# Optimization experiments

Measured on AMD Instinct MI355X. Metric: run time of the kernel, lower is better.

Reference implementation:

```python
import jax, jax.numpy as jnp
import numpy as np

N, E, B = 10000, 25000, 128
NF, EF, D = 32, 8, 64
STEPS = 3   # message passing steps
S2S = 3     # set2set processing steps
EPS = 1e-5

def setup_inputs() -> dict:
    key = jax.random.key(0)
    ks = jax.random.split(key, 32)
    g = lambda i, shape, scale=0.05: (jax.random.normal(ks[i], shape, dtype=jnp.float32) * scale)
    inp = {
        'x': jax.random.normal(ks[0], (N, NF), dtype=jnp.float32),
        'edge_index': jax.random.randint(ks[1], (2, E), 0, N, dtype=jnp.int32),
        'edge_attr': jax.random.normal(ks[2], (E, EF), dtype=jnp.float32),
        'batch': jnp.sort(jax.random.randint(ks[3], (N,), 0, B, dtype=jnp.int32)),
        # dense0
        'W0': g(4, (NF, D)), 'b0': jnp.zeros((D,), jnp.float32),
        # edge MLP: EF -> 2D -> D*D
        'We1': g(5, (EF, 2 * D)), 'be1': jnp.zeros((2 * D,), jnp.float32),
        'We2': g(6, (2 * D, D * D)), 'be2': jnp.zeros((D * D,), jnp.float32),
        # NNConv root weight + bias
        'root': g(7, (D, D)), 'conv_b': jnp.zeros((D,), jnp.float32),
        # GRU (input D, hidden D); gate order r, z, n (torch layout)
        'Wi': g(8, (D, 3 * D)), 'bi': jnp.zeros((3 * D,), jnp.float32),
        'Wh': g(9, (D, 3 * D)), 'bh': jnp.zeros((3 * D,), jnp.float32),
        # Set2Set LSTM (input 2D, hidden D); gate order i, f, g, o
        'Wli': g(10, (2 * D, 4 * D)), 'bli': jnp.zeros((4 * D,), jnp.float32),
        'Wlh': g(11, (D, 4 * D)), 'blh': jnp.zeros((4 * D,), jnp.float32),
        'Wr1': g(12, (2 * D, D)), 'br1': jnp.zeros((D,), jnp.float32),
        'gamma': jnp.ones((D,), jnp.float32), 'beta': jnp.zeros((D,), jnp.float32),
        'Wr2': g(13, (D, 1)), 'br2': jnp.zeros((1,), jnp.float32),
    }
    return inp

def _forward(x, edge_index, edge_attr, batch, W0, b0, We1, be1, We2, be2,
             root, conv_b, Wi, bi, Wh, bh, Wli, bli, Wlh, blh,
             Wr1, br1, gamma, beta, Wr2, br2):
    src, dst = edge_index[0], edge_index[1]
    out = jax.nn.relu(x @ W0 + b0)            # [N, D]
    h = out                                    # GRU hidden (seq_len=1)
    # edge-conditioned weights depend only on edge_attr -> compute once
    ew = (jax.nn.relu(edge_attr @ We1 + be1) @ We2 + be2).reshape(E, D, D)
    deg = jnp.maximum(jax.ops.segment_sum(jnp.ones((E,), x.dtype), dst, num_segments=N), 1.0)
    for _ in range(STEPS):
        msg = jnp.einsum('ed,edf->ef', out[src], ew)               # [E, D]
        agg = jax.ops.segment_sum(msg, dst, num_segments=N) / deg[:, None]
        m = jax.nn.relu(agg + out @ root + conv_b)                  # NNConv + relu
        # GRU cell
        gi = m @ Wi + bi
        gh = h @ Wh + bh
        ir, iz, ig = jnp.split(gi, 3, axis=-1)
        hr, hz, hg = jnp.split(gh, 3, axis=-1)
        r = jax.nn.sigmoid(ir + hr)
        z = jax.nn.sigmoid(iz + hz)
        n = jnp.tanh(ig + r * hg)
        h = (1.0 - z) * n + z * h
        out = h
    # Set2Set readout
    q_star = jnp.zeros((B, 2 * D), x.dtype)
    hl = jnp.zeros((B, D), x.dtype)
    cl = jnp.zeros((B, D), x.dtype)
    for _ in range(S2S):
        gates = q_star @ Wli + bli + hl @ Wlh + blh
        ig_, fg_, gg_, og_ = jnp.split(gates, 4, axis=-1)
        cl = jax.nn.sigmoid(fg_) * cl + jax.nn.sigmoid(ig_) * jnp.tanh(gg_)
        hl = jax.nn.sigmoid(og_) * jnp.tanh(cl)
        q = hl                                                      # [B, D]
        e = jnp.sum(out * q[batch], axis=-1)                        # [N]
        emax = jax.ops.segment_max(e, batch, num_segments=B)
        a = jnp.exp(e - emax[batch])
        a = a / jnp.maximum(jax.ops.segment_sum(a, batch, num_segments=B), 1e-12)[batch]
        r_read = jax.ops.segment_sum(a[:, None] * out, batch, num_segments=B)  # [B, D]
        q_star = jnp.concatenate([q, r_read], axis=-1)
    y = q_star @ Wr1 + br1
    mu = jnp.mean(y, axis=0)
    var = jnp.mean((y - mu) ** 2, axis=0)
    y = (y - mu) * jax.lax.rsqrt(var + EPS) * gamma + beta
    y = jax.nn.relu(y)
    y = y @ Wr2 + br2
    return y.reshape(-1)                                            # [B]

def reference(x, edge_index, edge_attr, batch, W0, b0, We1, be1, We2, be2,
              root, conv_b, Wi, bi, Wh, bh, Wli, bli, Wlh, blh,
              Wr1, br1, gamma, beta, Wr2, br2):
    return _forward(x, edge_index, edge_attr, batch, W0, b0, We1, be1, We2, be2,
                    root, conv_b, Wi, bi, Wh, bh, Wli, bli, Wlh, blh,
                    Wr1, br1, gamma, beta, Wr2, br2)
```

## Files before the change

kernel.cpp:

```cpp
#include <hip/hip_runtime.h>
#include <hip/hip_bf16.h>

constexpr int kN = 10000;
constexpr int kE = 25000;
constexpr int kB = 128;
constexpr int kNF = 32;
constexpr int kEF = 8;
constexpr int kD = 64;
constexpr int kGrp = 392;
constexpr int kEPad = kGrp * 64;
constexpr int kNCap = 320;

typedef __attribute__((ext_vector_type(8))) short short8;
typedef __attribute__((ext_vector_type(4))) float floatx4;
typedef __attribute__((ext_vector_type(16))) float floatx16;

__device__ __forceinline__ unsigned short f2bf(float f) {
  unsigned u = __float_as_uint(f);
  u = (u + 0x7fffu + ((u >> 16) & 1u)) >> 16;
  return (unsigned short)u;
}
__device__ __forceinline__ float sigmf(float x) { return 1.f / (1.f + __expf(-x)); }
__device__ __forceinline__ float tanh_(float x) { return 1.f - 2.f / (__expf(2.f * x) + 1.f); }

__device__ __forceinline__ unsigned cvtpk(float lo, float hi) {
  unsigned r;
  asm("v_cvt_pk_bf16_f32 %0, %1, %2" : "=v"(r) : "v"(lo), "v"(hi));
  return r;
}

constexpr int kBlkDense = 2500;
constexpr int kBlkHid   = 12544;
constexpr int kBlkPrep  = 258;
constexpr int kBlkDeg   = 98;
constexpr int kB0H = kBlkDense;
constexpr int kB0P = kB0H + kBlkHid;
constexpr int kB0G = kB0P + kBlkPrep;
constexpr int kB0B = kB0G + kBlkDeg;
constexpr int kBlkSetup = kB0B + 1;

__global__ __launch_bounds__(256) void k_setup(
    const float* __restrict__ x, const float* __restrict__ W0, const float* __restrict__ b0,
    const float* __restrict__ ea, const float* __restrict__ We1, const float* __restrict__ be1,
    const float* __restrict__ We2, const float* __restrict__ be2,
    const int* __restrict__ ei, const int* __restrict__ batch,
    float* __restrict__ outn, unsigned short* __restrict__ hid7,
    unsigned short* __restrict__ Bc2, float* __restrict__ deg, int* __restrict__ start) {
  const int blk = blockIdx.x, t = threadIdx.x;
  if (blk < kB0H) {
    int gid = blk * 256 + t;
    int n = gid >> 6, f = gid & 63;
    float acc = b0[f];
    const float* xr = x + n * kNF;
#pragma unroll
    for (int j = 0; j < kNF; ++j) acc += xr[j] * W0[j * kD + f];
    outn[gid] = fmaxf(acc, 0.f);
  } else if (blk < kB0P) {
    int gid = (blk - kB0H) * 256 + t;
    int e_loc = gid & 63, h = (gid >> 6) & 127, grp = gid >> 13;
    int e = grp * 64 + e_loc;
    float r = 0.f;
    if (e < kE) {
      float acc = be1[h];
      const float* er = ea + e * kEF;
#pragma unroll
      for (int j = 0; j < kEF; ++j) acc += er[j] * We1[j * 128 + h];
      r = fmaxf(acc, 0.f);
    }
    hid7[gid] = f2bf(r);
  } else if (blk < kB0G) {
    int lg = (blk - kB0P) * 256 + t;
    int lane = lg & 63, slot = lg >> 6;
    int fcol, dbase;
    const float* srcmat;
    if (slot < 1024) {
      int nf_ = slot & 1, hdb = slot >> 1;
      int db = hdb & 3, h = hdb >> 2;
      fcol = nf_ * 32 + (lane & 31);
      dbase = db * 16 + (lane >> 5) * 8;
      srcmat = We2 + (size_t)h * 4096;
    } else {
      int s = slot - 1024;
      int db = s >> 1, nf_ = s & 1;
      fcol = nf_ * 32 + (lane & 31);
      dbase = db * 16 + (lane >> 5) * 8;
      srcmat = be2;
    }
    unsigned short v[8];
#pragma unroll
    for (int j = 0; j < 8; ++j) v[j] = f2bf(srcmat[(size_t)(dbase + j) * 64 + fcol]);
    *(short8*)(Bc2 + (size_t)slot * 512 + lane * 8) = *(short8*)v;
  } else if (blk < kB0B) {
    int e = (blk - kB0G) * 256 + t;
    if (e < kE) atomicAdd(&deg[ei[kE + e]], 1.f);
  } else {
    if (t > kB) return;
    int lo = 0, hi = kN;
    while (lo < hi) { int mid = (lo + hi) >> 1; if (batch[mid] < t) lo = mid + 1; else hi = mid; }
    start[t] = lo;
  }
}

__global__ __launch_bounds__(256) void k_csr(const float* __restrict__ deg,
                                             int* __restrict__ ptr) {
  __shared__ int ps[256];
  int t = threadIdx.x;
  int base = t * 40;
  int s = 0;
#pragma unroll 8
  for (int j = 0; j < 40; ++j) {
    int n = base + j;
    if (n < kN) s += (int)deg[n];
  }
  ps[t] = s;
  __syncthreads();
  for (int off = 1; off < 256; off <<= 1) {
    int v = (t >= off) ? ps[t - off] : 0;
    __syncthreads();
    ps[t] += v;
    __syncthreads();
  }
  int run = ps[t] - s;
  for (int j = 0; j < 40; ++j) {
    int n = base + j;
    if (n < kN) { ptr[n] = run; run += (int)deg[n]; }
  }
  if (t == 255) ptr[kN] = ps[255];
}

__global__ __launch_bounds__(256) void k_scatter(const int* __restrict__ ei,
    const int* __restrict__ ptr, int* __restrict__ cnt, int* __restrict__ csr) {
  int e = blockIdx.x * 256 + threadIdx.x;
  if (e < kE) {
    int d = ei[kE + e];
    int pos = atomicAdd(&cnt[d], 1);
    csr[ptr[d] + pos] = e;
  }
}

__global__ __launch_bounds__(256) void k_msg7(const int* __restrict__ ei,
    const float* __restrict__ outn, const unsigned short* __restrict__ hid7,
    const unsigned short* __restrict__ Bc2,
    float* __restrict__ msg0, float* __restrict__ msg1) {
  __shared__ __align__(16) unsigned short hidS[64 * 64];
  __shared__ __align__(16) float res[4][64 * 64];
  const int t = threadIdx.x, lane = t & 63, wave = t >> 6;
  const int er = lane & 31, hi5 = lane >> 5;
  const int grp = blockIdx.x, by = blockIdx.y, e0 = grp * 64;
  float* __restrict__ msgP = by ? msg1 : msg0;
  {
    const char* hsrc = (const char*)(hid7 + (size_t)grp * 8192 + by * 4096);
#pragma unroll
    for (int i = 0; i < 2; ++i) {
      int off = (wave * 2 + i) * 1024 + lane * 16;
      __builtin_amdgcn_global_load_lds(
          (const __attribute__((address_space(1))) void*)(hsrc + off),
          (__attribute__((address_space(3))) void*)((char*)hidS + off), 16, 0, 0);
    }
  }
  const int hg0 = by * 64 + wave * 16;
  const unsigned short* bp = Bc2 + (size_t)(hg0 * 8) * 512 + lane * 8;
  short8 bvr[8];
#pragma unroll
  for (int j = 0; j < 8; ++j) bvr[j] = *(const short8*)(bp + (size_t)j * 512);
  floatx4 o[2][4][2];
#pragma unroll
  for (int mf = 0; mf < 2; ++mf) {
    int e = e0 + mf * 32 + er;
    int s = (e < kE) ? ei[e] : 0;
    const float* base = outn + (size_t)s * 64 + hi5 * 8;
#pragma unroll
    for (int db = 0; db < 4; ++db) {
      o[mf][db][0] = *(const floatx4*)(base + db * 16);
      o[mf][db][1] = *(const floatx4*)(base + db * 16 + 4);
    }
  }
  __syncthreads();

  floatx16 acc[2][2];
#pragma unroll
  for (int mf = 0; mf < 2; ++mf)
#pragma unroll
    for (int nf = 0; nf < 2; ++nf)
#pragma unroll
      for (int i = 0; i < 16; ++i) acc[mf][nf][i] = 0.f;

  const int hl0 = wave * 16;
#pragma unroll 2
  for (int hh = 0; hh < 16; ++hh) {
    int hl = hl0 + hh;
    float hv0 = __uint_as_float(((unsigned)hidS[hl * 64 + er]) << 16);
    float hv1 = __uint_as_float(((unsigned)hidS[hl * 64 + 32 + er]) << 16);
    const unsigned short* bpn = bp + (size_t)((hh + 1) * 8) * 512;
#pragma unroll
    for (int db = 0; db < 4; ++db) {
      short8 bv0 = bvr[db * 2], bv1 = bvr[db * 2 + 1];
      bvr[db * 2]     = *(const short8*)(bpn + (size_t)(db * 2) * 512);
      bvr[db * 2 + 1] = *(const short8*)(bpn + (size_t)(db * 2 + 1) * 512);
      union { uint4 u; short8 s; } U0, U1;
      floatx4 a0 = o[0][db][0] * hv0, b0 = o[0][db][1] * hv0;
      floatx4 a1 = o[1][db][0] * hv1, b1 = o[1][db][1] * hv1;
      U0.u.x = cvtpk(a0.x, a0.y); U0.u.y = cvtpk(a0.z, a0.w);
      U0.u.z = cvtpk(b0.x, b0.y); U0.u.w = cvtpk(b0.z, b0.w);
      U1.u.x = cvtpk(a1.x, a1.y); U1.u.y = cvtpk(a1.z, a1.w);
      U1.u.z = cvtpk(b1.x, b1.y); U1.u.w = cvtpk(b1.z, b1.w);
      acc[0][0] = __builtin_amdgcn_mfma_f32_32x32x16_bf16(U0.s, bv0, acc[0][0], 0, 0, 0);
      acc[0][1] = __builtin_amdgcn_mfma_f32_32x32x16_bf16(U0.s, bv1, acc[0][1], 0, 0, 0);
      acc[1][0] = __builtin_amdgcn_mfma_f32_32x32x16_bf16(U1.s, bv0, acc[1][0], 0, 0, 0);
      acc[1][1] = __builtin_amdgcn_mfma_f32_32x32x16_bf16(U1.s, bv1, acc[1][1], 0, 0, 0);
    }
  }
  if (by == 1 && wave == 3) {
#pragma unroll
    for (int db = 0; db < 4; ++db) {
      short8 bv0 = *(const short8*)(Bc2 + (size_t)(1024 + db * 2) * 512 + lane * 8);
      short8 bv1 = *(const short8*)(Bc2 + (size_t)(1024 + db * 2 + 1) * 512 + lane * 8);
      union { uint4 u; short8 s; } U0, U1;
      floatx4 a0 = o[0][db][0], b0 = o[0][db][1];
      floatx4 a1 = o[1][db][0], b1 = o[1][db][1];
      U0.u.x = cvtpk(a0.x, a0.y); U0.u.y = cvtpk(a0.z, a0.w);
      U0.u.z = cvtpk(b0.x, b0.y); U0.u.w = cvtpk(b0.z, b0.w);
      U1.u.x = cvtpk(a1.x, a1.y); U1.u.y = cvtpk(a1.z, a1.w);
      U1.u.z = cvtpk(b1.x, b1.y); U1.u.w = cvtpk(b1.z, b1.w);
      acc[0][0] = __builtin_amdgcn_mfma_f32_32x32x16_bf16(U0.s, bv0, acc[0][0], 0, 0, 0);
      acc[0][1] = __builtin_amdgcn_mfma_f32_32x32x16_bf16(U0.s, bv1, acc[0][1], 0, 0, 0);
      acc[1][0] = __builtin_amdgcn_mfma_f32_32x32x16_bf16(U1.s, bv0, acc[1][0], 0, 0, 0);
      acc[1][1] = __builtin_amdgcn_mfma_f32_32x32x16_bf16(U1.s, bv1, acc[1][1], 0, 0, 0);
    }
  }
#pragma unroll
  for (int mf = 0; mf < 2; ++mf)
#pragma unroll
    for (int nf = 0; nf < 2; ++nf)
#pragma unroll
      for (int reg = 0; reg < 16; ++reg) {
        int row = (reg & 3) + 8 * (reg >> 2) + 4 * hi5 + mf * 32;
        res[wave][row * 64 + nf * 32 + er] = acc[mf][nf][reg];
      }
  __syncthreads();
#pragma unroll
  for (int q = 0; q < 4; ++q) {
    int idx = q * 1024 + t * 4;
    float4 s4 = *(const float4*)&res[0][idx];
#pragma unroll
    for (int w = 1; w < 4; ++w) {
      float4 a4 = *(const float4*)&res[w][idx];
      s4.x += a4.x; s4.y += a4.y; s4.z += a4.z; s4.w += a4.w;
    }
    int e = e0 + (idx >> 6);
    if (e < kE) *(float4*)(msgP + (size_t)e * 64 + (idx & 63)) = s4;
  }
}

__global__ __launch_bounds__(256) void k_update(const float* __restrict__ msg0,
    const float* __restrict__ msg1, const int* __restrict__ ptr,
    const int* __restrict__ csr, const float* __restrict__ deg,
    const float* __restrict__ root, const float* __restrict__ convb,
    const float* __restrict__ Wi, const float* __restrict__ bi,
    const float* __restrict__ Wh, const float* __restrict__ bh,
    float* __restrict__ out) {
  __shared__ float sh_out[16][64];
  __shared__ float sh_m[16][64];
  int t = threadIdx.x, lane = t & 63, w = t >> 6;
  int nb = blockIdx.x * 16;
#pragma unroll
  for (int i = 0; i < 4; ++i) {
    int idx = t + i * 256;
    sh_out[idx >> 6][idx & 63] = out[(size_t)(nb + (idx >> 6)) * 64 + (idx & 63)];
  }
  __syncthreads();
  int n0 = w * 4;
  float acc[4];
#pragma unroll
  for (int i = 0; i < 4; ++i) {
    int n = nb + n0 + i;
    float dg = fmaxf(deg[n], 1.f);
    float s = 0.f;
    int p0 = ptr[n], p1 = ptr[n + 1];
    for (int k = p0; k < p1; ++k) {
      size_t off2 = (size_t)csr[k] * 64 + lane;
      s += msg0[off2] + msg1[off2];
    }
    acc[i] = s / dg + convb[lane];
  }
  for (int d = 0; d < 64; ++d) {
    float rv = root[d * 64 + lane];
#pragma unroll
    for (int i = 0; i < 4; ++i) acc[i] += sh_out[n0 + i][d] * rv;
  }
#pragma unroll
  for (int i = 0; i < 4; ++i) sh_m[n0 + i][lane] = fmaxf(acc[i], 0.f);
  __syncthreads();
  float ir[4] = {}, iz[4] = {}, ig[4] = {}, hr[4] = {}, hz[4] = {}, hg[4] = {};
  for (int d = 0; d < 64; ++d) {
    float wi0 = Wi[d * 192 + lane], wi1 = Wi[d * 192 + 64 + lane], wi2 = Wi[d * 192 + 128 + lane];
    float wh0 = Wh[d * 192 + lane], wh1 = Wh[d * 192 + 64 + lane], wh2 = Wh[d * 192 + 128 + lane];
#pragma unroll
    for (int i = 0; i < 4; ++i) {
      float mv = sh_m[n0 + i][d], hv = sh_out[n0 + i][d];
      ir[i] += mv * wi0; iz[i] += mv * wi1; ig[i] += mv * wi2;
      hr[i] += hv * wh0; hz[i] += hv * wh1; hg[i] += hv * wh2;
    }
  }
  float bi0 = bi[lane], bi1 = bi[64 + lane], bi2 = bi[128 + lane];
  float bh0 = bh[lane], bh1 = bh[64 + lane], bh2 = bh[128 + lane];
#pragma unroll
  for (int i = 0; i < 4; ++i) {
    float r = sigmf(ir[i] + bi0 + hr[i] + bh0);
    float z = sigmf(iz[i] + bi1 + hz[i] + bh1);
    float nn = tanh_(ig[i] + bi2 + r * (hg[i] + bh2));
    float h = sh_out[n0 + i][lane];
    out[(size_t)(nb + n0 + i) * 64 + lane] = (1.f - z) * nn + z * h;
  }
}

__global__ __launch_bounds__(256) void k_s2s3(const float* __restrict__ out,
    const int* __restrict__ start, const float* __restrict__ Wli,
    const float* __restrict__ bli, const float* __restrict__ Wlh,
    const float* __restrict__ blh, const float* __restrict__ Wr1,
    const float* __restrict__ br1, float* __restrict__ y1) {
  __shared__ float sno[kNCap * 65];
  __shared__ float ebuf[1024];
  __shared__ float qs[128], hls[64], cls[64], gates[256];
  __shared__ float part[4][64];
  __shared__ float sred[8];
  int b = blockIdx.x, t = threadIdx.x, lane = t & 63, w = t >> 6;
  int s0 = start[b], s1 = start[b + 1];
  int cnt = s1 - s0; if (cnt > 1024) cnt = 1024;
  int cstg = cnt < kNCap ? cnt : kNCap;
  for (int i = t; i < cstg * 64; i += 256)
    sno[(i >> 6) * 65 + (i & 63)] = out[(size_t)(s0 + (i >> 6)) * 64 + (i & 63)];
  if (t < 128) qs[t] = 0.f;
  if (t < 64) { hls[t] = 0.f; cls[t] = 0.f; }
  __syncthreads();
  for (int it = 0; it < 3; ++it) {
    float g = bli[t] + blh[t];
    for (int j = 0; j < 128; ++j) g += qs[j] * Wli[j * 256 + t];
    for (int j = 0; j < 64; ++j) g += hls[j] * Wlh[j * 256 + t];
    gates[t] = g;
    __syncthreads();
    if (t < 64) {
      float ig = sigmf(gates[t]), fg = sigmf(gates[64 + t]);
      float gg = tanh_(gates[128 + t]), og = sigmf(gates[192 + t]);
      float c = fg * cls[t] + ig * gg;
      float h = og * tanh_(c);
      cls[t] = c; hls[t] = h;
      qs[t] = h;
    }
    __syncthreads();
    for (int n = t; n < cnt; n += 256) {
      float e = 0.f;
      if (n < kNCap) {
        const float* row = &sno[n * 65];
#pragma unroll 16
        for (int d = 0; d < 64; ++d) e += row[d] * hls[d];
      } else {
        const float* row = out + (size_t)(s0 + n) * 64;
        for (int d = 0; d < 64; ++d) e += row[d] * hls[d];
      }
      ebuf[n] = e;
    }
    __syncthreads();
    float mx = -3.4e38f;
    for (int idx = t; idx < cnt; idx += 256) mx = fmaxf(mx, ebuf[idx]);
#pragma unroll
    for (int m = 1; m < 64; m <<= 1) mx = fmaxf(mx, __shfl_xor(mx, m, 64));
    if (lane == 0) sred[w] = mx;
    __syncthreads();
    mx = fmaxf(fmaxf(sred[0], sred[1]), fmaxf(sred[2], sred[3]));
    float s = 0.f;
    for (int idx = t; idx < cnt; idx += 256) {
      float a = __expf(ebuf[idx] - mx);
      ebuf[idx] = a; s += a;
    }
#pragma unroll
    for (int m = 1; m < 64; m <<= 1) s += __shfl_xor(s, m, 64);
    if (lane == 0) sred[4 + w] = s;
    __syncthreads();
    s = sred[4] + sred[5] + sred[6] + sred[7];
    float rs = 1.f / fmaxf(s, 1e-12f);
    float pr = 0.f;
    for (int n = w; n < cnt; n += 4) {
      float a = ebuf[n];
      pr += a * ((n < kNCap) ? sno[n * 65 + lane] : out[(size_t)(s0 + n) * 64 + lane]);
    }
    part[w][lane] = pr;
    __syncthreads();
    if (t < 64)
      qs[64 + t] = (part[0][t] + part[1][t] + part[2][t] + part[3][t]) * rs;
    __syncthreads();
  }
  if (t < 64) {
    float acc = br1[t];
    for (int j = 0; j < 128; ++j) acc += qs[j] * Wr1[j * 64 + t];
    y1[b * 64 + t] = acc;
  }
}

__global__ __launch_bounds__(256) void k_head2(const float* __restrict__ y1,
    const float* __restrict__ gamma, const float* __restrict__ beta,
    const float* __restrict__ Wr2, const float* __restrict__ br2,
    float* __restrict__ outp) {
  __shared__ float mu[64], ri[64];
  int t = threadIdx.x;
  if (t < 64) {
    float s1 = 0.f, s2 = 0.f;
    for (int b = 0; b < kB; ++b) { float v = y1[b * 64 + t]; s1 += v; s2 += v * v; }
    float m = s1 / (float)kB;
    mu[t] = m; ri[t] = rsqrtf(s2 / (float)kB - m * m + 1e-5f);
  }
  __syncthreads();
  if (t < kB) {
    float acc = br2[0];
    for (int f = 0; f < 64; ++f) {
      float v = (y1[t * 64 + f] - mu[f]) * ri[f] * gamma[f] + beta[f];
      acc += fmaxf(v, 0.f) * Wr2[f];
    }
    outp[t] = acc;
  }
}

extern "C" void kernel_launch(void* const* d_in, const int* in_sizes, int n_in,
                              void* d_out, int out_size, void* d_ws, size_t ws_size,
                              hipStream_t stream) {
  const float* x     = (const float*)d_in[0];
  const int*   ei    = (const int*)d_in[1];
  const float* ea    = (const float*)d_in[2];
  const int*   batch = (const int*)d_in[3];
  const float* W0    = (const float*)d_in[4];
  const float* b0    = (const float*)d_in[5];
  const float* We1   = (const float*)d_in[6];
  const float* be1   = (const float*)d_in[7];
  const float* We2   = (const float*)d_in[8];
  const float* be2   = (const float*)d_in[9];
  const float* root  = (const float*)d_in[10];
  const float* convb = (const float*)d_in[11];
  const float* Wi    = (const float*)d_in[12];
  const float* bi    = (const float*)d_in[13];
  const float* Wh    = (const float*)d_in[14];
  const float* bh    = (const float*)d_in[15];
  const float* Wli   = (const float*)d_in[16];
  const float* bli   = (const float*)d_in[17];
  const float* Wlh   = (const float*)d_in[18];
  const float* blh   = (const float*)d_in[19];
  const float* Wr1   = (const float*)d_in[20];
  const float* br1   = (const float*)d_in[21];
  const float* gamma = (const float*)d_in[22];
  const float* beta  = (const float*)d_in[23];
  const float* Wr2   = (const float*)d_in[24];
  const float* br2   = (const float*)d_in[25];
  (void)in_sizes; (void)n_in; (void)out_size; (void)ws_size;

  char* ws = (char*)d_ws;
  size_t off = 0;
  auto take = [&](size_t bytes) {
    char* p = ws + off;
    off += (bytes + 255) & ~(size_t)255;
    return p;
  };
  float* deg  = (float*)take((size_t)kN * 4);
  int*   cnt  = (int*)take((size_t)kN * 4);
  size_t zeroBytes = off;
  int*   ptr   = (int*)take((size_t)(kN + 1) * 4);
  int*   csr   = (int*)take((size_t)kE * 4);
  int*   start = (int*)take(256 * 4);
  float* outn  = (float*)take((size_t)kN * kD * 4);
  float* msg0  = (float*)take((size_t)kEPad * kD * 4);
  float* msg1  = (float*)take((size_t)kEPad * kD * 4);
  unsigned short* hid7 = (unsigned short*)take((size_t)kGrp * 8192 * 2);
  unsigned short* Bc2  = (unsigned short*)take((size_t)1032 * 512 * 2);
  float* y1    = (float*)take((size_t)kB * 64 * 4);

  hipMemsetAsync(deg, 0, zeroBytes, stream);
  k_setup<<<kBlkSetup, 256, 0, stream>>>(x, W0, b0, ea, We1, be1, We2, be2, ei, batch,
                                         outn, hid7, Bc2, deg, start);
  k_csr<<<1, 256, 0, stream>>>(deg, ptr);
  k_scatter<<<(kE + 255) / 256, 256, 0, stream>>>(ei, ptr, cnt, csr);
  dim3 gm(kGrp, 2);
  for (int s = 0; s < 3; ++s) {
    k_msg7<<<gm, 256, 0, stream>>>(ei, outn, hid7, Bc2, msg0, msg1);
    k_update<<<kN / 16, 256, 0, stream>>>(msg0, msg1, ptr, csr, deg, root, convb,
                                          Wi, bi, Wh, bh, outn);
  }
  k_s2s3<<<kB, 256, 0, stream>>>(outn, start, Wli, bli, Wlh, blh, Wr1, br1, y1);
  k_head2<<<1, 256, 0, stream>>>(y1, gamma, beta, Wr2, br2, (float*)d_out);
}
```

Before: 284.5 us.

## Switch edge-message MFMA to fp16 with packed half multiply and halve reduction LDS

The edge-message kernel now stores hidden activations and the We2/be2 tiles in fp16 instead of bf16. Source node features are converted to packed fp16 once, outside the loop, and each per-hidden scaling is a single packed half8 multiply rather than fp32 multiplies followed by bf16 pack conversions, which feeds f16 MFMA. The cross-wave reduction buffer is cut to half size by reducing the two 32-edge halves in sequence with extra barriers. Together these are meant to cut VALU conversion work in the inner loop and raise occupancy through lower LDS use, at the cost of fp16 range and rounding risks (round-toward-zero packing, products computed in half precision).

```diff
diff --git a/kernel.cpp b/kernel.cpp
--- a/kernel.cpp
+++ b/kernel.cpp
@@ -14,20 +14,22 @@
 typedef __attribute__((ext_vector_type(8))) short short8;
 typedef __attribute__((ext_vector_type(4))) float floatx4;
 typedef __attribute__((ext_vector_type(16))) float floatx16;
-
-__device__ __forceinline__ unsigned short f2bf(float f) {
-  unsigned u = __float_as_uint(f);
-  u = (u + 0x7fffu + ((u >> 16) & 1u)) >> 16;
-  return (unsigned short)u;
+typedef _Float16 half8 __attribute__((ext_vector_type(8)));
+
+union HU { uint4 u; half8 h; short8 s; };
+
+__device__ __forceinline__ unsigned short f2h(float f) {
+  union { _Float16 h; unsigned short u; } cv;
+  cv.h = (_Float16)f;
+  return cv.u;
+}
+__device__ __forceinline__ unsigned pkrtz(float lo, float hi) {
+  unsigned r;
+  asm("v_cvt_pkrtz_f16_f32 %0, %1, %2" : "=v"(r) : "v"(lo), "v"(hi));
+  return r;
 }
 __device__ __forceinline__ float sigmf(float x) { return 1.f / (1.f + __expf(-x)); }
 __device__ __forceinline__ float tanh_(float x) { return 1.f - 2.f / (__expf(2.f * x) + 1.f); }
-
-__device__ __forceinline__ unsigned cvtpk(float lo, float hi) {
-  unsigned r;
-  asm("v_cvt_pk_bf16_f32 %0, %1, %2" : "=v"(r) : "v"(lo), "v"(hi));
-  return r;
-}
 
 constexpr int kBlkDense = 2500;
 constexpr int kBlkHid   = 12544;
@@ -67,7 +69,7 @@
       for (int j = 0; j < kEF; ++j) acc += er[j] * We1[j * 128 + h];
       r = fmaxf(acc, 0.f);
     }
-    hid7[gid] = f2bf(r);
+    hid7[gid] = f2h(r);
   } else if (blk < kB0G) {
     int lg = (blk - kB0P) * 256 + t;
     int lane = lg & 63, slot = lg >> 6;
@@ -88,7 +90,7 @@
     }
     unsigned short v[8];
 #pragma unroll
-    for (int j = 0; j < 8; ++j) v[j] = f2bf(srcmat[(size_t)(dbase + j) * 64 + fcol]);
+    for (int j = 0; j < 8; ++j) v[j] = f2h(srcmat[(size_t)(dbase + j) * 64 + fcol]);
     *(short8*)(Bc2 + (size_t)slot * 512 + lane * 8) = *(short8*)v;
   } else if (blk < kB0B) {
     int e = (blk - kB0G) * 256 + t;
@@ -138,12 +140,12 @@
   }
 }
 
-__global__ __launch_bounds__(256) void k_msg7(const int* __restrict__ ei,
+__global__ __launch_bounds__(256) void k_msg8(const int* __restrict__ ei,
     const float* __restrict__ outn, const unsigned short* __restrict__ hid7,
     const unsigned short* __restrict__ Bc2,
     float* __restrict__ msg0, float* __restrict__ msg1) {
   __shared__ __align__(16) unsigned short hidS[64 * 64];
-  __shared__ __align__(16) float res[4][64 * 64];
+  __shared__ __align__(16) float res[4][32 * 64];
   const int t = threadIdx.x, lane = t & 63, wave = t >> 6;
   const int er = lane & 31, hi5 = lane >> 5;
   const int grp = blockIdx.x, by = blockIdx.y, e0 = grp * 64;
@@ -163,7 +165,7 @@
   short8 bvr[8];
 #pragma unroll
   for (int j = 0; j < 8; ++j) bvr[j] = *(const short8*)(bp + (size_t)j * 512);
-  floatx4 o[2][4][2];
+  HU o8[2][4];
 #pragma unroll
   for (int mf = 0; mf < 2; ++mf) {
     int e = e0 + mf * 32 + er;
@@ -171,8 +173,10 @@
     const float* base = outn + (size_t)s * 64 + hi5 * 8;
 #pragma unroll
     for (int db = 0; db < 4; ++db) {
-      o[mf][db][0] = *(const floatx4*)(base + db * 16);
-      o[mf][db][1] = *(const floatx4*)(base + db * 16 + 4);
+      floatx4 q0 = *(const floatx4*)(base + db * 16);
+      floatx4 q1 = *(const floatx4*)(base + db * 16 + 4);
+      o8[mf][db].u = (uint4){pkrtz(q0.x, q0.y), pkrtz(q0.z, q0.w),
+                             pkrtz(q1.x, q1.y), pkrtz(q1.z, q1.w)};
     }
   }
   __syncthreads();
@@ -189,66 +193,64 @@
 #pragma unroll 2
   for (int hh = 0; hh < 16; ++hh) {
     int hl = hl0 + hh;
-    float hv0 = __uint_as_float(((unsigned)hidS[hl * 64 + er]) << 16);
-    float hv1 = __uint_as_float(((unsigned)hidS[hl * 64 + 32 + er]) << 16);
+    unsigned p0 = (unsigned)hidS[hl * 64 + er] * 0x10001u;
+    unsigned p1 = (unsigned)hidS[hl * 64 + 32 + er] * 0x10001u;
+    HU hv0, hv1;
+    hv0.u = (uint4){p0, p0, p0, p0};
+    hv1.u = (uint4){p1, p1, p1, p1};
     const unsigned short* bpn = bp + (size_t)((hh + 1) * 8) * 512;
 #pragma unroll
     for (int db = 0; db < 4; ++db) {
-      short8 bv0 = bvr[db * 2], bv1 = bvr[db * 2 + 1];
+      HU bv0, bv1;
+      bv0.s = bvr[db * 2]; bv1.s = bvr[db * 2 + 1];
       bvr[db * 2]     = *(const short8*)(bpn + (size_t)(db * 2) * 512);
       bvr[db * 2 + 1] = *(const short8*)(bpn + (size_t)(db * 2 + 1) * 512);
-      union { uint4 u; short8 s; } U0, U1;
-      floatx4 a0 = o[0][db][0] * hv0, b0 = o[0][db][1] * hv0;
-      floatx4 a1 = o[1][db][0] * hv1, b1 = o[1][db][1] * hv1;
-      U0.u.x = cvtpk(a0.x, a0.y); U0.u.y = cvtpk(a0.z, a0.w);
-      U0.u.z = cvtpk(b0.x, b0.y); U0.u.w = cvtpk(b0.z, b0.w);
-      U1.u.x = cvtpk(a1.x, a1.y); U1.u.y = cvtpk(a1.z, a1.w);
-      U1.u.z = cvtpk(b1.x, b1.y); U1.u.w = cvtpk(b1.z, b1.w);
-      acc[0][0] = __builtin_amdgcn_mfma_f32_32x32x16_bf16(U0.s, bv0, acc[0][0], 0, 0, 0);
-      acc[0][1] = __builtin_amdgcn_mfma_f32_32x32x16_bf16(U0.s, bv1, acc[0][1], 0, 0, 0);
-      acc[1][0] = __builtin_amdgcn_mfma_f32_32x32x16_bf16(U1.s, bv0, acc[1][0], 0, 0, 0);
-      acc[1][1] = __builtin_amdgcn_mfma_f32_32x32x16_bf16(U1.s, bv1, acc[1][1], 0, 0, 0);
+      half8 a0 = o8[0][db].h * hv0.h;
+      half8 a1 = o8[1][db].h * hv1.h;
+      acc[0][0] = __builtin_amdgcn_mfma_f32_32x32x16_f16(a0, bv0.h, acc[0][0], 0, 0, 0);
+      acc[0][1] = __builtin_amdgcn_mfma_f32_32x32x16_f16(a0, bv1.h, acc[0][1], 0, 0, 0);
+      acc[1][0] = __builtin_amdgcn_mfma_f32_32x32x16_f16(a1, bv0.h, acc[1][0], 0, 0, 0);
+      acc[1][1] = __builtin_amdgcn_mfma_f32_32x32x16_f16(a1, bv1.h, acc[1][1], 0, 0, 0);
     }
   }
   if (by == 1 && wave == 3) {
 #pragma unroll
     for (int db = 0; db < 4; ++db) {
-      short8 bv0 = *(const short8*)(Bc2 + (size_t)(1024 + db * 2) * 512 + lane * 8);
-      short8 bv1 = *(const short8*)(Bc2 + (size_t)(1024 + db * 2 + 1) * 512 + lane * 8);
-      union { uint4 u; short8 s; } U0, U1;
-      floatx4 a0 = o[0][db][0], b0 = o[0][db][1];
-      floatx4 a1 = o[1][db][0], b1 = o[1][db][1];
-      U0.u.x = cvtpk(a0.x, a0.y); U0.u.y = cvtpk(a0.z, a0.w);
-      U0.u.z = cvtpk(b0.x, b0.y); U0.u.w = cvtpk(b0.z, b0.w);
-      U1.u.x = cvtpk(a1.x, a1.y); U1.u.y = cvtpk(a1.z, a1.w);
-      U1.u.z = cvtpk(b1.x, b1.y); U1.u.w = cvtpk(b1.z, b1.w);
-      acc[0][0] = __builtin_amdgcn_mfma_f32_32x32x16_bf16(U0.s, bv0, acc[0][0], 0, 0, 0);
-      acc[0][1] = __builtin_amdgcn_mfma_f32_32x32x16_bf16(U0.s, bv1, acc[0][1], 0, 0, 0);
-      acc[1][0] = __builtin_amdgcn_mfma_f32_32x32x16_bf16(U1.s, bv0, acc[1][0], 0, 0, 0);
-      acc[1][1] = __builtin_amdgcn_mfma_f32_32x32x16_bf16(U1.s, bv1, acc[1][1], 0, 0, 0);
-    }
-  }
-#pragma unroll
-  for (int mf = 0; mf < 2; ++mf)
+      HU bv0, bv1;
+      bv0.s = *(const short8*)(Bc2 + (size_t)(1024 + db * 2) * 512 + lane * 8);
+      bv1.s = *(const short8*)(Bc2 + (size_t)(1024 + db * 2 + 1) * 512 + lane * 8);
+      acc[0][0] = __builtin_amdgcn_mfma_f32_32x32x16_f16(o8[0][db].h, bv0.h, acc[0][0], 0, 0, 0);
+      acc[0][1] = __builtin_amdgcn_mfma_f32_32x32x16_f16(o8[0][db].h, bv1.h, acc[0][1], 0, 0, 0);
+      acc[1][0] = __builtin_amdgcn_mfma_f32_32x32x16_f16(o8[1][db].h, bv0.h, acc[1][0], 0, 0, 0);
+      acc[1][1] = __builtin_amdgcn_mfma_f32_32x32x16_f16(o8[1][db].h, bv1.h, acc[1][1], 0, 0, 0);
+    }
+  }
+#pragma unroll
+  for (int mf = 0; mf < 2; ++mf) {
 #pragma unroll
     for (int nf = 0; nf < 2; ++nf)
 #pragma unroll
       for (int reg = 0; reg < 16; ++reg) {
-        int row = (reg & 3) + 8 * (reg >> 2) + 4 * hi5 + mf * 32;
+        int row = (reg & 3) + 8 * (reg >> 2) + 4 * hi5;
         res[wave][row * 64 + nf * 32 + er] = acc[mf][nf][reg];
       }
-  __syncthreads();
-#pragma unroll
-  for (int q = 0; q < 4; ++q) {
-    int idx = q * 1024 + t * 4;
-    float4 s4 = *(const float4*)&res[0][idx];
+    __syncthreads();
+    int r = t >> 3, fo = (t & 7) * 8;
+    float4 sA = *(const float4*)&res[0][r * 64 + fo];
+    float4 sB = *(const float4*)&res[0][r * 64 + fo + 4];
 #pragma unroll
     for (int w = 1; w < 4; ++w) {
-      float4 a4 = *(const float4*)&res[w][idx];
-      s4.x += a4.x; s4.y += a4.y; s4.z += a4.z; s4.w += a4.w;
-    }
-    int e = e0 + (idx >> 6);
-    if (e < kE) *(float4*)(msgP + (size_t)e * 64 + (idx & 63)) = s4;
+      float4 aA = *(const float4*)&res[w][r * 64 + fo];
+      float4 aB = *(const float4*)&res[w][r * 64 + fo + 4];
+      sA.x += aA.x; sA.y += aA.y; sA.z += aA.z; sA.w += aA.w;
+      sB.x += aB.x; sB.y += aB.y; sB.z += aB.z; sB.w += aB.w;
+    }
+    int e = e0 + mf * 32 + r;
+    if (e < kE) {
+      *(float4*)(msgP + (size_t)e * 64 + fo) = sA;
+      *(float4*)(msgP + (size_t)e * 64 + fo + 4) = sB;
+    }
+    __syncthreads();
   }
 }
 
@@ -478,7 +480,7 @@
   k_scatter<<<(kE + 255) / 256, 256, 0, stream>>>(ei, ptr, cnt, csr);
   dim3 gm(kGrp, 2);
   for (int s = 0; s < 3; ++s) {
-    k_msg7<<<gm, 256, 0, stream>>>(ei, outn, hid7, Bc2, msg0, msg1);
+    k_msg8<<<gm, 256, 0, stream>>>(ei, outn, hid7, Bc2, msg0, msg1);
     k_update<<<kN / 16, 256, 0, stream>>>(msg0, msg1, ptr, csr, deg, root, convb,
                                           Wi, bi, Wh, bh, outn);
   }
```

Result: no change. 285.1 us (+0.2%).
